# Kernel tuning notes

Hardware: AMD Instinct MI355X
Metric: run time of the kernel (lower is better)

Reference implementation:

```python
import jax, jax.numpy as jnp
import numpy as np

TOP_K = 2
NORM_TOPK = True


def setup_inputs() -> dict:
    key = jax.random.key(0)
    k1, k2, k3, k4 = jax.random.split(key, 4)
    B, S, H = 2, 1024, 2048
    E, I = 16, 768
    hidden_states = jax.random.normal(k1, (B, S, H), dtype=jnp.float32)
    gate_w = jax.random.normal(k2, (E, H), dtype=jnp.float32) * 0.02
    gate_up_w = jax.random.normal(k3, (E, 2 * I, H), dtype=jnp.float32) * 0.02
    down_w = jax.random.normal(k4, (E, H, I), dtype=jnp.float32) * 0.02
    return {
        "hidden_states": hidden_states,
        "gate_w": gate_w,
        "gate_up_w": gate_up_w,
        "down_w": down_w,
        "top_k": TOP_K,
    }


def reference(hidden_states, gate_w, gate_up_w, down_w, top_k):
    B, S, H = hidden_states.shape
    E = gate_w.shape[0]
    x = hidden_states.reshape(-1, H)  # [T, H]
    T = x.shape[0]

    # Router: softmax in float32 (as in torch F.softmax(..., dtype=torch.float))
    router_logits = x @ gate_w.T  # [T, E]
    probs = jax.nn.softmax(router_logits.astype(jnp.float32), axis=-1)
    top_w, top_idx = jax.lax.top_k(probs, top_k)  # [T, k]
    if NORM_TOPK:
        top_w = top_w / jnp.sum(top_w, axis=-1, keepdims=True)
    top_w = top_w.astype(x.dtype)

    # Dense combine weights [T, E]: routing weight where selected, 0 elsewhere.
    comb = jnp.sum(jax.nn.one_hot(top_idx, E, dtype=x.dtype) * top_w[..., None], axis=1)

    # SwiGLU expert MLPs evaluated for all experts, combined with sparse weights.
    gu = jnp.einsum("th,efh->tef", x, gate_up_w)  # [T, E, 2I]
    g, u = jnp.split(gu, 2, axis=-1)
    h = jax.nn.silu(g) * u  # [T, E, I]
    y = jnp.einsum("tei,ehi->teh", h, down_w)  # [T, E, H]
    out = jnp.einsum("teh,te->th", y, comb)  # [T, H]

    return out.reshape(B, S, H), router_logits
```

## Files before the change

### kernel.cpp

```cpp
#include <hip/hip_runtime.h>
#include <hip/hip_bf16.h>
#include <stdint.h>

#define T_TOK 2048
#define H_DIM 2048
#define E_NUM 16
#define I_DIM 768

typedef __bf16 bf16;
typedef __bf16 bf16x8 __attribute__((ext_vector_type(8)));
typedef float f32x4 __attribute__((ext_vector_type(4)));

__device__ __forceinline__ void async_cp16(bf16* l, const bf16* g) {
    __builtin_amdgcn_global_load_lds(
        (const __attribute__((address_space(1))) void*)g,
        (__attribute__((address_space(3))) void*)l, 16, 0, 0);
}

__global__ __launch_bounds__(256) void router_kernel(
    const float* __restrict__ x, const float* __restrict__ gw,
    float* __restrict__ logits, int* __restrict__ cnt,
    int* __restrict__ tok_list, float* __restrict__ wgt_list,
    bf16* __restrict__ xb)
{
    int t = blockIdx.x;
    int tid = threadIdx.x;
    __shared__ double red[E_NUM][256];
    double part[E_NUM];
#pragma unroll
    for (int e = 0; e < E_NUM; ++e) part[e] = 0.0;
    for (int h = tid; h < H_DIM; h += 256) {
        float xf = x[(size_t)t * H_DIM + h];
        xb[(size_t)t * H_DIM + h] = (bf16)xf;
        double xv = (double)xf;
#pragma unroll
        for (int e = 0; e < E_NUM; ++e)
            part[e] += xv * (double)gw[e * H_DIM + h];
    }
#pragma unroll
    for (int e = 0; e < E_NUM; ++e) red[e][tid] = part[e];
    __syncthreads();
    for (int s = 128; s > 0; s >>= 1) {
        if (tid < s) {
#pragma unroll
            for (int e = 0; e < E_NUM; ++e) red[e][tid] += red[e][tid + s];
        }
        __syncthreads();
    }
    __shared__ float lg[E_NUM];
    if (tid < E_NUM) {
        float v = (float)red[tid][0];
        lg[tid] = v;
        logits[(size_t)t * E_NUM + tid] = v;
    }
    __syncthreads();
    if (tid == 0) {
        int i0 = 0; float v0 = lg[0];
#pragma unroll
        for (int e = 1; e < E_NUM; ++e) if (lg[e] > v0) { v0 = lg[e]; i0 = e; }
        int i1 = -1; float v1 = -3.4e38f;
#pragma unroll
        for (int e = 0; e < E_NUM; ++e) if (e != i0 && lg[e] > v1) { v1 = lg[e]; i1 = e; }
        float w0 = 1.0f / (1.0f + __expf(v1 - v0));
        float w1 = 1.0f - w0;
        int p0 = atomicAdd(&cnt[i0], 1);
        tok_list[i0 * T_TOK + p0] = t; wgt_list[i0 * T_TOK + p0] = w0;
        int p1 = atomicAdd(&cnt[i1], 1);
        tok_list[i1 * T_TOK + p1] = t; wgt_list[i1 * T_TOK + p1] = w1;
    }
}

__global__ void scan_kernel(const int* __restrict__ cnt, int* __restrict__ offs)
{
    if (threadIdx.x == 0) {
        int o = 0;
        for (int e = 0; e < E_NUM; ++e) { offs[e] = o; o += cnt[e]; }
    }
}

__global__ __launch_bounds__(256) void convert_kernel(
    const float* __restrict__ gup, const float* __restrict__ dwn,
    bf16* __restrict__ gub, bf16* __restrict__ dwb)
{
    const size_t NG = (size_t)E_NUM * 2 * I_DIM * H_DIM / 8;
    const size_t ND = (size_t)E_NUM * H_DIM * I_DIM / 8;
    size_t stride = (size_t)gridDim.x * 256;
    for (size_t c = (size_t)blockIdx.x * 256 + threadIdx.x; c < NG + ND; c += stride) {
        const float* s; bf16* d; size_t off;
        if (c < NG) { s = gup; d = gub; off = c * 8; }
        else        { s = dwn; d = dwb; off = (c - NG) * 8; }
        float4 a = *(const float4*)(s + off);
        float4 b = *(const float4*)(s + off + 4);
        bf16x8 v = { (bf16)a.x, (bf16)a.y, (bf16)a.z, (bf16)a.w,
                     (bf16)b.x, (bf16)b.y, (bf16)b.z, (bf16)b.w };
        *(bf16x8*)(d + off) = v;
    }
}

__global__ __launch_bounds__(256, 4) void gateup_kernel(
    const bf16* __restrict__ xb, const bf16* __restrict__ gub,
    const int* __restrict__ cnt, const int* __restrict__ offs,
    const int* __restrict__ tok_list, bf16* __restrict__ hbuf)
{
    const int e = blockIdx.z;
    const int count = cnt[e];
    const int row0 = blockIdx.y * 64;
    if (row0 >= count) return;
    const int i0 = blockIdx.x * 64;
    const int hoff = offs[e];
    const int tid = threadIdx.x;

    __shared__ __align__(16) bf16 As[64 * 64];
    __shared__ __align__(16) bf16 Bs[128 * 64];
    __shared__ int toks[64];

    if (tid < 64) {
        int r = row0 + tid; if (r >= count) r = count - 1;
        toks[tid] = tok_list[e * T_TOK + r];
    }
    __syncthreads();

    const int lane = tid & 63, wid = tid >> 6;
    const int la = lane & 15, lq = lane >> 4;
    const int wm = wid >> 1, wn = wid & 1;

    int ra0 = tid >> 3, s0 = tid & 7;
    int ca0 = s0 ^ (ra0 & 7);
    int ra1 = ra0 + 32;
    int ca1 = s0 ^ (ra1 & 7);
    const bf16* srcA0 = xb + (size_t)toks[ra0] * H_DIM + ca0 * 8;
    const bf16* srcA1 = xb + (size_t)toks[ra1] * H_DIM + ca1 * 8;
    bf16* dstA0 = As + (size_t)(wid * 64) * 8;
    bf16* dstA1 = As + (size_t)(wid * 64 + 256) * 8;

    const bf16* srcB[4]; bf16* dstB[4];
#pragma unroll
    for (int i = 0; i < 4; ++i) {
        int idx = tid + 256 * i;
        int r = idx >> 3, s = idx & 7;
        int c8 = s ^ (r & 7);
        int is_u = (r >> 5) & 1;
        int ioff = (r >> 6) * 32 + (r & 31);
        size_t grow = (size_t)e * (2 * I_DIM) + (size_t)is_u * I_DIM + i0 + ioff;
        srcB[i] = gub + grow * H_DIM + c8 * 8;
        dstB[i] = Bs + (size_t)(256 * i + wid * 64) * 8;
    }

    f32x4 acc[2][4];
#pragma unroll
    for (int a = 0; a < 2; ++a)
#pragma unroll
        for (int b = 0; b < 4; ++b) acc[a][b] = (f32x4){0.f, 0.f, 0.f, 0.f};

    for (int k0 = 0; k0 < H_DIM; k0 += 64) {
        async_cp16(dstA0, srcA0 + k0);
        async_cp16(dstA1, srcA1 + k0);
#pragma unroll
        for (int i = 0; i < 4; ++i) async_cp16(dstB[i], srcB[i] + k0);
        __syncthreads();
#pragma unroll
        for (int ks = 0; ks < 2; ++ks) {
            bf16x8 af[2], bfr[4];
            int ch = lq + 4 * ks;
#pragma unroll
            for (int mt = 0; mt < 2; ++mt) {
                int row = 32 * wm + 16 * mt + la;
                int sl = ch ^ (row & 7);
                af[mt] = *(const bf16x8*)(As + (size_t)(row * 8 + sl) * 8);
            }
#pragma unroll
            for (int nt = 0; nt < 4; ++nt) {
                int row = 64 * wn + 16 * nt + la;
                int sl = ch ^ (row & 7);
                bfr[nt] = *(const bf16x8*)(Bs + (size_t)(row * 8 + sl) * 8);
            }
#pragma unroll
            for (int mt = 0; mt < 2; ++mt)
#pragma unroll
                for (int nt = 0; nt < 4; ++nt)
                    acc[mt][nt] = __builtin_amdgcn_mfma_f32_16x16x32_bf16(af[mt], bfr[nt], acc[mt][nt], 0, 0, 0);
        }
        __syncthreads();
    }

#pragma unroll
    for (int mt = 0; mt < 2; ++mt)
#pragma unroll
        for (int p = 0; p < 2; ++p)
#pragma unroll
            for (int r = 0; r < 4; ++r) {
                int trow = 32 * wm + 16 * mt + lq * 4 + r;
                if (row0 + trow < count) {
                    float g = acc[mt][p][r], u = acc[mt][p + 2][r];
                    float hv = (g / (1.0f + __expf(-g))) * u;
                    int col = i0 + 32 * wn + 16 * p + la;
                    hbuf[(size_t)(hoff + row0 + trow) * I_DIM + col] = (bf16)hv;
                }
            }
}

__global__ __launch_bounds__(256, 4) void down_kernel(
    const bf16* __restrict__ dwb, const bf16* __restrict__ hbuf,
    const int* __restrict__ cnt, const int* __restrict__ offs,
    const int* __restrict__ tok_list, const float* __restrict__ wgt_list,
    float* __restrict__ out)
{
    const int e = blockIdx.z;
    const int count = cnt[e];
    const int row0 = blockIdx.y * 64;
    if (row0 >= count) return;
    const int n0 = blockIdx.x * 128;
    const int hoff = offs[e];
    const int tid = threadIdx.x;

    __shared__ __align__(16) bf16 As[64 * 64];
    __shared__ __align__(16) bf16 Bs[128 * 64];
    __shared__ int toks[64];
    __shared__ float wgts[64];

    if (tid < 64) {
        int r = row0 + tid; if (r >= count) r = count - 1;
        toks[tid] = tok_list[e * T_TOK + r];
        wgts[tid] = wgt_list[e * T_TOK + r];
    }
    __syncthreads();

    const int lane = tid & 63, wid = tid >> 6;
    const int la = lane & 15, lq = lane >> 4;
    const int wm = wid >> 1, wn = wid & 1;

    int ra0 = tid >> 3, s0 = tid & 7;
    int ca0 = s0 ^ (ra0 & 7);
    int ra1 = ra0 + 32;
    int ca1 = s0 ^ (ra1 & 7);
    int ar0 = row0 + ra0; if (ar0 >= count) ar0 = count - 1;
    int ar1 = row0 + ra1; if (ar1 >= count) ar1 = count - 1;
    const bf16* srcA0 = hbuf + (size_t)(hoff + ar0) * I_DIM + ca0 * 8;
    const bf16* srcA1 = hbuf + (size_t)(hoff + ar1) * I_DIM + ca1 * 8;
    bf16* dstA0 = As + (size_t)(wid * 64) * 8;
    bf16* dstA1 = As + (size_t)(wid * 64 + 256) * 8;

    const bf16* srcB[4]; bf16* dstB[4];
#pragma unroll
    for (int i = 0; i < 4; ++i) {
        int idx = tid + 256 * i;
        int r = idx >> 3, s = idx & 7;
        int c8 = s ^ (r & 7);
        srcB[i] = dwb + ((size_t)e * H_DIM + n0 + r) * I_DIM + c8 * 8;
        dstB[i] = Bs + (size_t)(256 * i + wid * 64) * 8;
    }

    f32x4 acc[2][4];
#pragma unroll
    for (int a = 0; a < 2; ++a)
#pragma unroll
        for (int b = 0; b < 4; ++b) acc[a][b] = (f32x4){0.f, 0.f, 0.f, 0.f};

    for (int k0 = 0; k0 < I_DIM; k0 += 64) {
        async_cp16(dstA0, srcA0 + k0);
        async_cp16(dstA1, srcA1 + k0);
#pragma unroll
        for (int i = 0; i < 4; ++i) async_cp16(dstB[i], srcB[i] + k0);
        __syncthreads();
#pragma unroll
        for (int ks = 0; ks < 2; ++ks) {
            bf16x8 af[2], bfr[4];
            int ch = lq + 4 * ks;
#pragma unroll
            for (int mt = 0; mt < 2; ++mt) {
                int row = 32 * wm + 16 * mt + la;
                int sl = ch ^ (row & 7);
                af[mt] = *(const bf16x8*)(As + (size_t)(row * 8 + sl) * 8);
            }
#pragma unroll
            for (int nt = 0; nt < 4; ++nt) {
                int row = 64 * wn + 16 * nt + la;
                int sl = ch ^ (row & 7);
                bfr[nt] = *(const bf16x8*)(Bs + (size_t)(row * 8 + sl) * 8);
            }
#pragma unroll
            for (int mt = 0; mt < 2; ++mt)
#pragma unroll
                for (int nt = 0; nt < 4; ++nt)
                    acc[mt][nt] = __builtin_amdgcn_mfma_f32_16x16x32_bf16(af[mt], bfr[nt], acc[mt][nt], 0, 0, 0);
        }
        __syncthreads();
    }

#pragma unroll
    for (int mt = 0; mt < 2; ++mt)
#pragma unroll
        for (int nt = 0; nt < 4; ++nt)
#pragma unroll
            for (int r = 0; r < 4; ++r) {
                int trow = 32 * wm + 16 * mt + lq * 4 + r;
                if (row0 + trow < count) {
                    int col = n0 + 64 * wn + 16 * nt + la;
                    atomicAdd(&out[(size_t)toks[trow] * H_DIM + col],
                              wgts[trow] * acc[mt][nt][r]);
                }
            }
}

extern "C" void kernel_launch(void* const* d_in, const int* in_sizes, int n_in,
                              void* d_out, int out_size, void* d_ws, size_t ws_size,
                              hipStream_t stream)
{
    const float* x   = (const float*)d_in[0];
    const float* gw  = (const float*)d_in[1];
    const float* gup = (const float*)d_in[2];
    const float* dw  = (const float*)d_in[3];
    float* out = (float*)d_out;
    float* logits = out + (size_t)T_TOK * H_DIM;

    char* ws = (char*)d_ws;
    int*   cnt      = (int*)(ws + 0);
    int*   offs     = (int*)(ws + 256);
    int*   tok_list = (int*)(ws + 512);
    float* wgt_list = (float*)(ws + 131584);
    bf16*  hbuf     = (bf16*)(ws + 262656);
    bf16*  xb       = (bf16*)(ws + 6554112);
    bf16*  gub      = (bf16*)(ws + 14942720);
    bf16*  dwb      = (bf16*)(ws + 115606016);

    hipMemsetAsync(cnt, 0, 256, stream);
    hipMemsetAsync(out, 0, (size_t)T_TOK * H_DIM * sizeof(float), stream);

    convert_kernel<<<4096, 256, 0, stream>>>(gup, dw, gub, dwb);
    router_kernel<<<T_TOK, 256, 0, stream>>>(x, gw, logits, cnt, tok_list, wgt_list, xb);
    scan_kernel<<<1, 64, 0, stream>>>(cnt, offs);
    gateup_kernel<<<dim3(I_DIM / 64, T_TOK / 64, E_NUM), 256, 0, stream>>>(
        xb, gub, cnt, offs, tok_list, hbuf);
    down_kernel<<<dim3(H_DIM / 128, T_TOK / 64, E_NUM), 256, 0, stream>>>(
        dwb, hbuf, cnt, offs, tok_list, wgt_list, out);
}
```

Before: 555.5 us.

## Fuse weight bf16 conversion into GEMM loads and use shuffle reduction in router

```diff
diff --git a/kernel.cpp b/kernel.cpp
--- a/kernel.cpp
+++ b/kernel.cpp
@@ -8,10 +8,11 @@
 #define I_DIM 768
 
 typedef __bf16 bf16;
+typedef __bf16 bf16x4 __attribute__((ext_vector_type(4)));
 typedef __bf16 bf16x8 __attribute__((ext_vector_type(8)));
 typedef float f32x4 __attribute__((ext_vector_type(4)));
 
-__device__ __forceinline__ void async_cp16(bf16* l, const bf16* g) {
+__device__ __forceinline__ void async_cp16(void* l, const void* g) {
     __builtin_amdgcn_global_load_lds(
         (const __attribute__((address_space(1))) void*)g,
         (__attribute__((address_space(3))) void*)l, 16, 0, 0);
@@ -23,33 +24,41 @@
     int* __restrict__ tok_list, float* __restrict__ wgt_list,
     bf16* __restrict__ xb)
 {
-    int t = blockIdx.x;
-    int tid = threadIdx.x;
-    __shared__ double red[E_NUM][256];
+    const int t = blockIdx.x;
+    const int tid = threadIdx.x;
+    const int lane = tid & 63, wid = tid >> 6;
+
     double part[E_NUM];
 #pragma unroll
     for (int e = 0; e < E_NUM; ++e) part[e] = 0.0;
-    for (int h = tid; h < H_DIM; h += 256) {
-        float xf = x[(size_t)t * H_DIM + h];
-        xb[(size_t)t * H_DIM + h] = (bf16)xf;
-        double xv = (double)xf;
+
+#pragma unroll
+    for (int it = 0; it < 2; ++it) {
+        int h = it * 1024 + tid * 4;
+        float4 xv = *(const float4*)(x + (size_t)t * H_DIM + h);
+        bf16x4 xb4 = { (bf16)xv.x, (bf16)xv.y, (bf16)xv.z, (bf16)xv.w };
+        *(bf16x4*)(xb + (size_t)t * H_DIM + h) = xb4;
+#pragma unroll
+        for (int e = 0; e < E_NUM; ++e) {
+            float4 wv = *(const float4*)(gw + (size_t)e * H_DIM + h);
+            part[e] += (double)xv.x * (double)wv.x + (double)xv.y * (double)wv.y
+                     + (double)xv.z * (double)wv.z + (double)xv.w * (double)wv.w;
+        }
+    }
+#pragma unroll
+    for (int off = 32; off > 0; off >>= 1)
 #pragma unroll
         for (int e = 0; e < E_NUM; ++e)
-            part[e] += xv * (double)gw[e * H_DIM + h];
-    }
-#pragma unroll
-    for (int e = 0; e < E_NUM; ++e) red[e][tid] = part[e];
+            part[e] += __shfl_down(part[e], off);
+
+    __shared__ double sh[4][E_NUM];
+    __shared__ float lg[E_NUM];
+    if (lane == 0)
+#pragma unroll
+        for (int e = 0; e < E_NUM; ++e) sh[wid][e] = part[e];
     __syncthreads();
-    for (int s = 128; s > 0; s >>= 1) {
-        if (tid < s) {
-#pragma unroll
-            for (int e = 0; e < E_NUM; ++e) red[e][tid] += red[e][tid + s];
-        }
-        __syncthreads();
-    }
-    __shared__ float lg[E_NUM];
     if (tid < E_NUM) {
-        float v = (float)red[tid][0];
+        float v = (float)(sh[0][tid] + sh[1][tid] + sh[2][tid] + sh[3][tid]);
         lg[tid] = v;
         logits[(size_t)t * E_NUM + tid] = v;
     }
@@ -78,27 +87,8 @@
     }
 }
 
-__global__ __launch_bounds__(256) void convert_kernel(
-    const float* __restrict__ gup, const float* __restrict__ dwn,
-    bf16* __restrict__ gub, bf16* __restrict__ dwb)
-{
-    const size_t NG = (size_t)E_NUM * 2 * I_DIM * H_DIM / 8;
-    const size_t ND = (size_t)E_NUM * H_DIM * I_DIM / 8;
-    size_t stride = (size_t)gridDim.x * 256;
-    for (size_t c = (size_t)blockIdx.x * 256 + threadIdx.x; c < NG + ND; c += stride) {
-        const float* s; bf16* d; size_t off;
-        if (c < NG) { s = gup; d = gub; off = c * 8; }
-        else        { s = dwn; d = dwb; off = (c - NG) * 8; }
-        float4 a = *(const float4*)(s + off);
-        float4 b = *(const float4*)(s + off + 4);
-        bf16x8 v = { (bf16)a.x, (bf16)a.y, (bf16)a.z, (bf16)a.w,
-                     (bf16)b.x, (bf16)b.y, (bf16)b.z, (bf16)b.w };
-        *(bf16x8*)(d + off) = v;
-    }
-}
-
 __global__ __launch_bounds__(256, 4) void gateup_kernel(
-    const bf16* __restrict__ xb, const bf16* __restrict__ gub,
+    const bf16* __restrict__ xb, const float* __restrict__ gup,
     const int* __restrict__ cnt, const int* __restrict__ offs,
     const int* __restrict__ tok_list, bf16* __restrict__ hbuf)
 {
@@ -109,41 +99,33 @@
     const int i0 = blockIdx.x * 64;
     const int hoff = offs[e];
     const int tid = threadIdx.x;
+    const int lane = tid & 63, wid = tid >> 6;
 
     __shared__ __align__(16) bf16 As[64 * 64];
-    __shared__ __align__(16) bf16 Bs[128 * 64];
-    __shared__ int toks[64];
-
-    if (tid < 64) {
-        int r = row0 + tid; if (r >= count) r = count - 1;
-        toks[tid] = tok_list[e * T_TOK + r];
-    }
-    __syncthreads();
-
-    const int lane = tid & 63, wid = tid >> 6;
-    const int la = lane & 15, lq = lane >> 4;
-    const int wm = wid >> 1, wn = wid & 1;
-
-    int ra0 = tid >> 3, s0 = tid & 7;
-    int ca0 = s0 ^ (ra0 & 7);
-    int ra1 = ra0 + 32;
-    int ca1 = s0 ^ (ra1 & 7);
-    const bf16* srcA0 = xb + (size_t)toks[ra0] * H_DIM + ca0 * 8;
-    const bf16* srcA1 = xb + (size_t)toks[ra1] * H_DIM + ca1 * 8;
+    __shared__ __align__(16) float Bs[128 * 64];
+
+    int raA0 = tid >> 3, sA0 = tid & 7;
+    int raA1 = raA0 + 32;
+    int cA0 = sA0 ^ (raA0 & 7);
+    int cA1 = sA0 ^ (raA1 & 7);
+    int tr0 = row0 + raA0; if (tr0 >= count) tr0 = count - 1;
+    int tr1 = row0 + raA1; if (tr1 >= count) tr1 = count - 1;
+    const bf16* srcA0 = xb + (size_t)tok_list[e * T_TOK + tr0] * H_DIM + cA0 * 8;
+    const bf16* srcA1 = xb + (size_t)tok_list[e * T_TOK + tr1] * H_DIM + cA1 * 8;
     bf16* dstA0 = As + (size_t)(wid * 64) * 8;
     bf16* dstA1 = As + (size_t)(wid * 64 + 256) * 8;
 
-    const bf16* srcB[4]; bf16* dstB[4];
-#pragma unroll
-    for (int i = 0; i < 4; ++i) {
-        int idx = tid + 256 * i;
-        int r = idx >> 3, s = idx & 7;
-        int c8 = s ^ (r & 7);
+    const float* srcB[8]; float* dstB[8];
+#pragma unroll
+    for (int i = 0; i < 8; ++i) {
+        int idx = i * 256 + tid;
+        int r = idx >> 4, s = idx & 15;
+        int c = s ^ (r & 15);
         int is_u = (r >> 5) & 1;
         int ioff = (r >> 6) * 32 + (r & 31);
         size_t grow = (size_t)e * (2 * I_DIM) + (size_t)is_u * I_DIM + i0 + ioff;
-        srcB[i] = gub + grow * H_DIM + c8 * 8;
-        dstB[i] = Bs + (size_t)(256 * i + wid * 64) * 8;
+        srcB[i] = gup + grow * H_DIM + c * 4;
+        dstB[i] = Bs + (size_t)(i * 256 + wid * 64) * 4;
     }
 
     f32x4 acc[2][4];
@@ -151,28 +133,36 @@
     for (int a = 0; a < 2; ++a)
 #pragma unroll
         for (int b = 0; b < 4; ++b) acc[a][b] = (f32x4){0.f, 0.f, 0.f, 0.f};
+
+    const int la = lane & 15, lq = lane >> 4;
+    const int wm = wid >> 1, wn = wid & 1;
 
     for (int k0 = 0; k0 < H_DIM; k0 += 64) {
         async_cp16(dstA0, srcA0 + k0);
         async_cp16(dstA1, srcA1 + k0);
 #pragma unroll
-        for (int i = 0; i < 4; ++i) async_cp16(dstB[i], srcB[i] + k0);
+        for (int i = 0; i < 8; ++i) async_cp16(dstB[i], srcB[i] + k0);
         __syncthreads();
 #pragma unroll
         for (int ks = 0; ks < 2; ++ks) {
             bf16x8 af[2], bfr[4];
-            int ch = lq + 4 * ks;
+            int chA = ks * 4 + lq;
+            int c0 = ks * 8 + lq * 2;
 #pragma unroll
             for (int mt = 0; mt < 2; ++mt) {
                 int row = 32 * wm + 16 * mt + la;
-                int sl = ch ^ (row & 7);
+                int sl = chA ^ (row & 7);
                 af[mt] = *(const bf16x8*)(As + (size_t)(row * 8 + sl) * 8);
             }
 #pragma unroll
             for (int nt = 0; nt < 4; ++nt) {
                 int row = 64 * wn + 16 * nt + la;
-                int sl = ch ^ (row & 7);
-                bfr[nt] = *(const bf16x8*)(Bs + (size_t)(row * 8 + sl) * 8);
+                int s0 = c0 ^ (row & 15);
+                int s1 = s0 ^ 1;
+                f32x4 v0 = *(const f32x4*)(Bs + (size_t)(row * 16 + s0) * 4);
+                f32x4 v1 = *(const f32x4*)(Bs + (size_t)(row * 16 + s1) * 4);
+                bfr[nt] = (bf16x8){ (bf16)v0.x, (bf16)v0.y, (bf16)v0.z, (bf16)v0.w,
+                                    (bf16)v1.x, (bf16)v1.y, (bf16)v1.z, (bf16)v1.w };
             }
 #pragma unroll
             for (int mt = 0; mt < 2; ++mt)
@@ -200,7 +190,7 @@
 }
 
 __global__ __launch_bounds__(256, 4) void down_kernel(
-    const bf16* __restrict__ dwb, const bf16* __restrict__ hbuf,
+    const float* __restrict__ dw, const bf16* __restrict__ hbuf,
     const int* __restrict__ cnt, const int* __restrict__ offs,
     const int* __restrict__ tok_list, const float* __restrict__ wgt_list,
     float* __restrict__ out)
@@ -212,71 +202,67 @@
     const int n0 = blockIdx.x * 128;
     const int hoff = offs[e];
     const int tid = threadIdx.x;
+    const int lane = tid & 63, wid = tid >> 6;
 
     __shared__ __align__(16) bf16 As[64 * 64];
-    __shared__ __align__(16) bf16 Bs[128 * 64];
-    __shared__ int toks[64];
-    __shared__ float wgts[64];
-
-    if (tid < 64) {
-        int r = row0 + tid; if (r >= count) r = count - 1;
-        toks[tid] = tok_list[e * T_TOK + r];
-        wgts[tid] = wgt_list[e * T_TOK + r];
-    }
-    __syncthreads();
-
-    const int lane = tid & 63, wid = tid >> 6;
+    __shared__ __align__(16) float Bs[128 * 64];
+
+    int raA0 = tid >> 3, sA0 = tid & 7;
+    int raA1 = raA0 + 32;
+    int cA0 = sA0 ^ (raA0 & 7);
+    int cA1 = sA0 ^ (raA1 & 7);
+    int ar0 = row0 + raA0; if (ar0 >= count) ar0 = count - 1;
+    int ar1 = row0 + raA1; if (ar1 >= count) ar1 = count - 1;
+    const bf16* srcA0 = hbuf + (size_t)(hoff + ar0) * I_DIM + cA0 * 8;
+    const bf16* srcA1 = hbuf + (size_t)(hoff + ar1) * I_DIM + cA1 * 8;
+    bf16* dstA0 = As + (size_t)(wid * 64) * 8;
+    bf16* dstA1 = As + (size_t)(wid * 64 + 256) * 8;
+
+    const float* srcB[8]; float* dstB[8];
+#pragma unroll
+    for (int i = 0; i < 8; ++i) {
+        int idx = i * 256 + tid;
+        int r = idx >> 4, s = idx & 15;
+        int c = s ^ (r & 15);
+        srcB[i] = dw + ((size_t)e * H_DIM + n0 + r) * I_DIM + c * 4;
+        dstB[i] = Bs + (size_t)(i * 256 + wid * 64) * 4;
+    }
+
+    f32x4 acc[2][4];
+#pragma unroll
+    for (int a = 0; a < 2; ++a)
+#pragma unroll
+        for (int b = 0; b < 4; ++b) acc[a][b] = (f32x4){0.f, 0.f, 0.f, 0.f};
+
     const int la = lane & 15, lq = lane >> 4;
     const int wm = wid >> 1, wn = wid & 1;
-
-    int ra0 = tid >> 3, s0 = tid & 7;
-    int ca0 = s0 ^ (ra0 & 7);
-    int ra1 = ra0 + 32;
-    int ca1 = s0 ^ (ra1 & 7);
-    int ar0 = row0 + ra0; if (ar0 >= count) ar0 = count - 1;
-    int ar1 = row0 + ra1; if (ar1 >= count) ar1 = count - 1;
-    const bf16* srcA0 = hbuf + (size_t)(hoff + ar0) * I_DIM + ca0 * 8;
-    const bf16* srcA1 = hbuf + (size_t)(hoff + ar1) * I_DIM + ca1 * 8;
-    bf16* dstA0 = As + (size_t)(wid * 64) * 8;
-    bf16* dstA1 = As + (size_t)(wid * 64 + 256) * 8;
-
-    const bf16* srcB[4]; bf16* dstB[4];
-#pragma unroll
-    for (int i = 0; i < 4; ++i) {
-        int idx = tid + 256 * i;
-        int r = idx >> 3, s = idx & 7;
-        int c8 = s ^ (r & 7);
-        srcB[i] = dwb + ((size_t)e * H_DIM + n0 + r) * I_DIM + c8 * 8;
-        dstB[i] = Bs + (size_t)(256 * i + wid * 64) * 8;
-    }
-
-    f32x4 acc[2][4];
-#pragma unroll
-    for (int a = 0; a < 2; ++a)
-#pragma unroll
-        for (int b = 0; b < 4; ++b) acc[a][b] = (f32x4){0.f, 0.f, 0.f, 0.f};
 
     for (int k0 = 0; k0 < I_DIM; k0 += 64) {
         async_cp16(dstA0, srcA0 + k0);
         async_cp16(dstA1, srcA1 + k0);
 #pragma unroll
-        for (int i = 0; i < 4; ++i) async_cp16(dstB[i], srcB[i] + k0);
+        for (int i = 0; i < 8; ++i) async_cp16(dstB[i], srcB[i] + k0);
         __syncthreads();
 #pragma unroll
         for (int ks = 0; ks < 2; ++ks) {
             bf16x8 af[2], bfr[4];
-            int ch = lq + 4 * ks;
+            int chA = ks * 4 + lq;
+            int c0 = ks * 8 + lq * 2;
 #pragma unroll
             for (int mt = 0; mt < 2; ++mt) {
                 int row = 32 * wm + 16 * mt + la;
-                int sl = ch ^ (row & 7);
+                int sl = chA ^ (row & 7);
                 af[mt] = *(const bf16x8*)(As + (size_t)(row * 8 + sl) * 8);
             }
 #pragma unroll
             for (int nt = 0; nt < 4; ++nt) {
                 int row = 64 * wn + 16 * nt + la;
-                int sl = ch ^ (row & 7);
-                bfr[nt] = *(const bf16x8*)(Bs + (size_t)(row * 8 + sl) * 8);
+                int s0 = c0 ^ (row & 15);
+                int s1 = s0 ^ 1;
+                f32x4 v0 = *(const f32x4*)(Bs + (size_t)(row * 16 + s0) * 4);
+                f32x4 v1 = *(const f32x4*)(Bs + (size_t)(row * 16 + s1) * 4);
+                bfr[nt] = (bf16x8){ (bf16)v0.x, (bf16)v0.y, (bf16)v0.z, (bf16)v0.w,
+                                    (bf16)v1.x, (bf16)v1.y, (bf16)v1.z, (bf16)v1.w };
             }
 #pragma unroll
             for (int mt = 0; mt < 2; ++mt)
@@ -296,8 +282,9 @@
                 int trow = 32 * wm + 16 * mt + lq * 4 + r;
                 if (row0 + trow < count) {
                     int col = n0 + 64 * wn + 16 * nt + la;
-                    atomicAdd(&out[(size_t)toks[trow] * H_DIM + col],
-                              wgts[trow] * acc[mt][nt][r]);
+                    int grow = row0 + trow;
+                    atomicAdd(&out[(size_t)tok_list[e * T_TOK + grow] * H_DIM + col],
+                              wgt_list[e * T_TOK + grow] * acc[mt][nt][r]);
                 }
             }
 }
@@ -320,17 +307,14 @@
     float* wgt_list = (float*)(ws + 131584);
     bf16*  hbuf     = (bf16*)(ws + 262656);
     bf16*  xb       = (bf16*)(ws + 6554112);
-    bf16*  gub      = (bf16*)(ws + 14942720);
-    bf16*  dwb      = (bf16*)(ws + 115606016);
 
     hipMemsetAsync(cnt, 0, 256, stream);
     hipMemsetAsync(out, 0, (size_t)T_TOK * H_DIM * sizeof(float), stream);
 
-    convert_kernel<<<4096, 256, 0, stream>>>(gup, dw, gub, dwb);
     router_kernel<<<T_TOK, 256, 0, stream>>>(x, gw, logits, cnt, tok_list, wgt_list, xb);
     scan_kernel<<<1, 64, 0, stream>>>(cnt, offs);
     gateup_kernel<<<dim3(I_DIM / 64, T_TOK / 64, E_NUM), 256, 0, stream>>>(
-        xb, gub, cnt, offs, tok_list, hbuf);
+        xb, gup, cnt, offs, tok_list, hbuf);
     down_kernel<<<dim3(H_DIM / 128, T_TOK / 64, E_NUM), 256, 0, stream>>>(
-        dwb, hbuf, cnt, offs, tok_list, wgt_list, out);
-}
+        dw, hbuf, cnt, offs, tok_list, wgt_list, out);
+}
```

Result: faster. 529.8 us (-4.6%).
